# Optimization experiments

Hardware: AMD Instinct MI355X
Metric: run time of the kernel (lower is better)

Reference implementation:

```python
import jax, jax.numpy as jnp
import numpy as np

H = 512  # hidden/input size
T = 16384
CLAMP_MAX = 49688.0

def setup_inputs() -> dict:
    key = jax.random.key(0)
    ks = jax.random.split(key, 12)
    s = 0.05
    x = jax.random.normal(ks[0], (T, 1, H), dtype=jnp.float32)
    W_ih = jax.random.normal(ks[1], (4 * H, H), dtype=jnp.float32) * s
    W_hh = jax.random.normal(ks[2], (4 * H, H), dtype=jnp.float32) * s
    b_ih = jax.random.normal(ks[3], (4 * H,), dtype=jnp.float32) * s
    b_hh = jax.random.normal(ks[4], (4 * H,), dtype=jnp.float32) * s
    fc_w = jax.random.normal(ks[5], (128, H), dtype=jnp.float32) * s
    fc_b = jax.random.normal(ks[6], (128,), dtype=jnp.float32) * s
    fc1_w = jax.random.normal(ks[7], (16, 128), dtype=jnp.float32) * s
    fc1_b = jax.random.normal(ks[8], (16,), dtype=jnp.float32) * s
    fc2_w = jax.random.normal(ks[9], (37, 128), dtype=jnp.float32) * s
    fc2_b = jax.random.normal(ks[10], (37,), dtype=jnp.float32) * s
    return {"x": x, "W_ih": W_ih, "W_hh": W_hh, "b_ih": b_ih, "b_hh": b_hh,
            "fc_w": fc_w, "fc_b": fc_b, "fc1_w": fc1_w, "fc1_b": fc1_b,
            "fc2_w": fc2_w, "fc2_b": fc2_b}

def _lstm(x, W_ih, W_hh, b_ih, b_hh):
    # x: [T, 1, H] seq-major, batch=1. Precompute input contribution for all t.
    xf = x.reshape(-1, H)                       # [T, H]
    x_gates = xf @ W_ih.T + (b_ih + b_hh)       # [T, 4H]

    def step(carry, xg):
        h, c = carry                            # [H], [H]
        g = xg + W_hh @ h                       # [4H]
        i = jax.nn.sigmoid(g[:H])
        f = jax.nn.sigmoid(g[H:2 * H])
        gg = jnp.tanh(g[2 * H:3 * H])
        o = jax.nn.sigmoid(g[3 * H:])
        c = f * c + i * gg
        h = o * jnp.tanh(c)
        return (h, c), h

    h0 = jnp.zeros((H,), dtype=x.dtype)
    c0 = jnp.zeros((H,), dtype=x.dtype)
    _, hs = jax.lax.scan(step, (h0, c0), x_gates)  # hs: [T, H]
    return hs

def reference(x, W_ih, W_hh, b_ih, b_hh, fc_w, fc_b, fc1_w, fc1_b, fc2_w, fc2_b):
    hs = _lstm(x, W_ih, W_hh, b_ih, b_hh)       # [T, H]
    inter = hs @ fc_w.T + fc_b                  # [T, 128]
    action = jnp.clip(inter @ fc1_w.T + fc1_b, 0.0, CLAMP_MAX)  # [T, 16]
    obj = jnp.clip(inter @ fc2_w.T + fc2_b, 0.0, CLAMP_MAX)     # [T, 37]
    return (action, obj)
```

## Files before the change

kernel.cpp:

```cpp
#include <hip/hip_runtime.h>
#include <hip/hip_bf16.h>
#include <stdint.h>

#define T_LEN 16384
#define HDIM 512
#define G4 2048
#define CLAMP_MAXV 49688.0f

#define XG_OFF    0ull
#define HS_OFF    134217728ull
#define INTER_OFF 167772160ull
#define HREC_OFF  176160768ull
#define BSUM_OFF  176168960ull
#define WS_NEED   176177152ull

__global__ __launch_bounds__(256) void init_k(uint64_t* __restrict__ hrec,
                                              const float* __restrict__ b_ih,
                                              const float* __restrict__ b_hh,
                                              float* __restrict__ bsum) {
    int i = blockIdx.x * 256 + threadIdx.x;
    if (i < 1024) hrec[i] = 0ull;
    bsum[i] = b_ih[i] + b_hh[i];
}

__global__ __launch_bounds__(256) void gemm_abt(const float* __restrict__ A,
                                                const float* __restrict__ B,
                                                const float* __restrict__ bias,
                                                float* __restrict__ C,
                                                int N, int K) {
    __shared__ float As[16][68];
    __shared__ float Bs[16][68];
    const int tid = threadIdx.x;
    const int bm = blockIdx.x << 6, bn = blockIdx.y << 6;
    const int tx = tid & 15, ty = tid >> 4;
    const int lr = tid >> 2, lk = (tid & 3) << 2;
    float acc[4][4] = {};
    const float* Ap = A + (size_t)(bm + lr) * K + lk;
    const float* Bp = B + (size_t)(bn + lr) * K + lk;
    for (int kt = 0; kt < K; kt += 16) {
        float4 av = *(const float4*)(Ap + kt);
        float4 bv = *(const float4*)(Bp + kt);
        __syncthreads();
        As[lk + 0][lr] = av.x; As[lk + 1][lr] = av.y;
        As[lk + 2][lr] = av.z; As[lk + 3][lr] = av.w;
        Bs[lk + 0][lr] = bv.x; Bs[lk + 1][lr] = bv.y;
        Bs[lk + 2][lr] = bv.z; Bs[lk + 3][lr] = bv.w;
        __syncthreads();
#pragma unroll
        for (int kk = 0; kk < 16; ++kk) {
            float4 a4 = *(const float4*)&As[kk][ty << 2];
            float4 b4 = *(const float4*)&Bs[kk][tx << 2];
            acc[0][0] += a4.x * b4.x; acc[0][1] += a4.x * b4.y;
            acc[0][2] += a4.x * b4.z; acc[0][3] += a4.x * b4.w;
            acc[1][0] += a4.y * b4.x; acc[1][1] += a4.y * b4.y;
            acc[1][2] += a4.y * b4.z; acc[1][3] += a4.y * b4.w;
            acc[2][0] += a4.z * b4.x; acc[2][1] += a4.z * b4.y;
            acc[2][2] += a4.z * b4.z; acc[2][3] += a4.z * b4.w;
            acc[3][0] += a4.w * b4.x; acc[3][1] += a4.w * b4.y;
            acc[3][2] += a4.w * b4.z; acc[3][3] += a4.w * b4.w;
        }
    }
    const int col = bn + (tx << 2);
    float4 bv4 = *(const float4*)&bias[col];
#pragma unroll
    for (int i = 0; i < 4; ++i) {
        int row = bm + (ty << 2) + i;
        float4 o;
        o.x = acc[i][0] + bv4.x; o.y = acc[i][1] + bv4.y;
        o.z = acc[i][2] + bv4.z; o.w = acc[i][3] + bv4.w;
        *(float4*)&C[(size_t)row * N + col] = o;
    }
}

__global__ __launch_bounds__(512, 2) void lstm_scan(const float* __restrict__ W_hh,
                                                    const float* __restrict__ xg,
                                                    float* __restrict__ hs,
                                                    uint64_t* __restrict__ hrec) {
    __shared__ __align__(16) float h_lds[512];
    __shared__ float part[2][512];
    const int tid = threadIdx.x;
    const int wv = tid >> 6;
    const int lane = tid & 63;
    const int j = blockIdx.x;
    const int rowg = ((lane >> 4) << 9) | (j << 4) | (lane & 15);

    float4 w4[16];
    {
        const float4* wp = (const float4*)(W_hh + (size_t)rowg * HDIM + (wv << 6));
#pragma unroll
        for (int q = 0; q < 16; ++q) w4[q] = wp[q];
    }

    float c_reg = 0.f;
    for (int t = 0; t < T_LEN; ++t) {
        float xgv = 0.f;
        if (wv == 0) xgv = xg[(size_t)t * G4 + rowg];

        uint64_t* src = hrec + ((t & 1) << 9) + tid;
        uint64_t a0 = __hip_atomic_load(src, __ATOMIC_RELAXED, __HIP_MEMORY_SCOPE_AGENT);
        uint64_t a1 = __hip_atomic_load(src, __ATOMIC_RELAXED, __HIP_MEMORY_SCOPE_AGENT);
        int guard = 0;
        while ((uint32_t)(a0 >> 32) != (uint32_t)t && ++guard < (1 << 18)) {
            a0 = a1;
            a1 = __hip_atomic_load(src, __ATOMIC_RELAXED, __HIP_MEMORY_SCOPE_AGENT);
        }
        h_lds[tid] = __uint_as_float((uint32_t)a0);
        __builtin_amdgcn_wave_barrier();

        float ac0 = 0.f, ac1 = 0.f, ac2 = 0.f, ac3 = 0.f;
        const float* hp = h_lds + (wv << 6);
#pragma unroll
        for (int q = 0; q < 16; q += 4) {
            float4 h0 = *(const float4*)(hp + (q << 2));
            float4 h1 = *(const float4*)(hp + ((q + 1) << 2));
            float4 h2 = *(const float4*)(hp + ((q + 2) << 2));
            float4 h3 = *(const float4*)(hp + ((q + 3) << 2));
            ac0 += w4[q].x * h0.x + w4[q].y * h0.y + w4[q].z * h0.z + w4[q].w * h0.w;
            ac1 += w4[q + 1].x * h1.x + w4[q + 1].y * h1.y + w4[q + 1].z * h1.z + w4[q + 1].w * h1.w;
            ac2 += w4[q + 2].x * h2.x + w4[q + 2].y * h2.y + w4[q + 2].z * h2.z + w4[q + 2].w * h2.w;
            ac3 += w4[q + 3].x * h3.x + w4[q + 3].y * h3.y + w4[q + 3].z * h3.z + w4[q + 3].w * h3.w;
        }
        float v = (ac0 + ac1) + (ac2 + ac3);
        if (wv) part[t & 1][tid] = v;
        __syncthreads();

        if (wv == 0) {
            float g = xgv + v;
            const float* pp = part[t & 1];
#pragma unroll
            for (int ww = 1; ww < 8; ++ww) g += pp[(ww << 6) | lane];
            bool isg = (lane >= 32) && (lane < 48);
            float y = isg ? (g + g) : g;
            float s = 1.f / (1.f + __expf(-y));
            float a = isg ? (s + s - 1.f) : s;
            float fa = __shfl_down(a, 16);
            float ga = __shfl_down(a, 32);
            float oa = __shfl_down(a, 48);
            if (lane < 16) {
                c_reg = fa * c_reg + a * ga;
                float e2 = __expf(-2.f * c_reg);
                float hv = oa * (2.f / (1.f + e2) - 1.f);
                uint64_t pu = ((uint64_t)(uint32_t)(t + 1) << 32) |
                              (uint64_t)__float_as_uint(hv);
                __hip_atomic_store(hrec + (((t + 1) & 1) << 9) + (j << 4) + lane, pu,
                                   __ATOMIC_RELAXED, __HIP_MEMORY_SCOPE_AGENT);
                hs[(size_t)t * HDIM + (j << 4) + lane] = hv;
            }
        }
    }
}

__global__ __launch_bounds__(256) void heads_k(const float* __restrict__ inter,
                                               const float* __restrict__ fc1w,
                                               const float* __restrict__ fc1b,
                                               const float* __restrict__ fc2w,
                                               const float* __restrict__ fc2b,
                                               float* __restrict__ out) {
    __shared__ float it[64][128];
    __shared__ float wt[128][56];
    __shared__ float bl[56];
    const int tid = threadIdx.x;
    const int t0 = blockIdx.x << 6;
    for (int q = tid; q < 64 * 32; q += 256) {
        int r = q >> 5, c4 = q & 31;
        *(float4*)&it[r][c4 << 2] =
            *(const float4*)&inter[(size_t)(t0 + r) * 128 + (c4 << 2)];
    }
    for (int q = tid; q < 53 * 32; q += 256) {
        int r = q >> 5, c4 = q & 31;
        float4 v = (r < 16) ? ((const float4*)&fc1w[r * 128])[c4]
                            : ((const float4*)&fc2w[(r - 16) * 128])[c4];
        int k = c4 << 2;
        wt[k + 0][r] = v.x; wt[k + 1][r] = v.y; wt[k + 2][r] = v.z; wt[k + 3][r] = v.w;
    }
    if (tid < 53) bl[tid] = (tid < 16) ? fc1b[tid] : fc2b[tid - 16];
    __syncthreads();
    const int c = tid & 63, rg = tid >> 6;
    if (c < 53) {
        float b = bl[c];
        for (int rr = 0; rr < 16; ++rr) {
            int r = (rg << 4) + rr;
            float acc = b;
#pragma unroll 8
            for (int k = 0; k < 128; k += 4) {
                float4 iv = *(const float4*)&it[r][k];
                acc += iv.x * wt[k][c] + iv.y * wt[k + 1][c] +
                       iv.z * wt[k + 2][c] + iv.w * wt[k + 3][c];
            }
            acc = fminf(fmaxf(acc, 0.f), CLAMP_MAXV);
            int t = t0 + r;
            if (c < 16) out[(size_t)t * 16 + c] = acc;
            else        out[262144 + (size_t)t * 37 + (c - 16)] = acc;
        }
    }
}

extern "C" void kernel_launch(void* const* d_in, const int* in_sizes, int n_in,
                              void* d_out, int out_size, void* d_ws, size_t ws_size,
                              hipStream_t stream) {
    const float* x     = (const float*)d_in[0];
    const float* W_ih  = (const float*)d_in[1];
    const float* W_hh  = (const float*)d_in[2];
    const float* b_ih  = (const float*)d_in[3];
    const float* b_hh  = (const float*)d_in[4];
    const float* fc_w  = (const float*)d_in[5];
    const float* fc_b  = (const float*)d_in[6];
    const float* fc1_w = (const float*)d_in[7];
    const float* fc1_b = (const float*)d_in[8];
    const float* fc2_w = (const float*)d_in[9];
    const float* fc2_b = (const float*)d_in[10];

    if (ws_size < WS_NEED) return;

    char* ws = (char*)d_ws;
    float*    xg    = (float*)(ws + XG_OFF);
    float*    hs    = (float*)(ws + HS_OFF);
    float*    inter = (float*)(ws + INTER_OFF);
    uint64_t* hrec  = (uint64_t*)(ws + HREC_OFF);
    float*    bsum  = (float*)(ws + BSUM_OFF);
    float*    out   = (float*)d_out;

    hipLaunchKernelGGL(init_k, dim3(8), dim3(256), 0, stream, hrec, b_ih, b_hh, bsum);
    hipLaunchKernelGGL(gemm_abt, dim3(256, 32), dim3(256), 0, stream,
                       x, W_ih, bsum, xg, 2048, 512);
    hipLaunchKernelGGL(lstm_scan, dim3(32), dim3(512), 0, stream, W_hh, xg, hs, hrec);
    hipLaunchKernelGGL(gemm_abt, dim3(256, 2), dim3(256), 0, stream,
                       hs, fc_w, fc_b, inter, 128, 512);
    hipLaunchKernelGGL(heads_k, dim3(256), dim3(256), 0, stream,
                       inter, fc1_w, fc1_b, fc2_w, fc2_b, out);
}
```

Measured before the change: 23.12 ms.

## Prefetch xg via helper wave, batch hs stores, reduce partials with LDS atomics

Wave 1 now prefetches the input-gate rows two steps ahead into a double-buffered LDS slot, so wave 0 no longer waits on a global load in the serial recurrence. The hs writes move off wave 0: values are staged in LDS and written by wave 2 every four steps. The cross-wave partial sums are combined with LDS atomicAdd into a 64-entry buffer instead of wave 0 reading seven partials serially. This shortens the per-step critical path, at the cost of atomic contention on LDS and a possible ordering race on the staged hs buffer, which has no block barrier between wave 0's write and wave 2's read.

```diff
diff --git a/kernel.cpp b/kernel.cpp
--- a/kernel.cpp
+++ b/kernel.cpp
@@ -77,7 +77,9 @@
                                                     float* __restrict__ hs,
                                                     uint64_t* __restrict__ hrec) {
     __shared__ __align__(16) float h_lds[512];
-    __shared__ float part[2][512];
+    __shared__ float part[2][64];
+    __shared__ float xg_lds[2][64];
+    __shared__ float hv_lds[64];
     const int tid = threadIdx.x;
     const int wv = tid >> 6;
     const int lane = tid & 63;
@@ -91,11 +93,16 @@
         for (int q = 0; q < 16; ++q) w4[q] = wp[q];
     }
 
+    if (tid < 128) ((float*)part)[tid] = 0.f;
+    float xg_inflight = 0.f;
+    if (wv == 1) {
+        xg_lds[0][lane] = xg[rowg];
+        xg_inflight = xg[(size_t)G4 + rowg];
+    }
+    __syncthreads();
+
     float c_reg = 0.f;
     for (int t = 0; t < T_LEN; ++t) {
-        float xgv = 0.f;
-        if (wv == 0) xgv = xg[(size_t)t * G4 + rowg];
-
         uint64_t* src = hrec + ((t & 1) << 9) + tid;
         uint64_t a0 = __hip_atomic_load(src, __ATOMIC_RELAXED, __HIP_MEMORY_SCOPE_AGENT);
         uint64_t a1 = __hip_atomic_load(src, __ATOMIC_RELAXED, __HIP_MEMORY_SCOPE_AGENT);
@@ -106,6 +113,20 @@
         }
         h_lds[tid] = __uint_as_float((uint32_t)a0);
         __builtin_amdgcn_wave_barrier();
+
+        float xgv = 0.f;
+        if (wv == 0) {
+            xgv = xg_lds[t & 1][lane];
+        } else if (wv == 1) {
+            xg_lds[(t + 1) & 1][lane] = xg_inflight;
+            int i2 = (t + 2 < T_LEN) ? (t + 2) : (T_LEN - 1);
+            xg_inflight = xg[(size_t)i2 * G4 + rowg];
+        } else if (wv == 2) {
+            if ((t & 3) == 0 && t > 0) {
+                float hvv = hv_lds[lane];
+                hs[(size_t)(t - 4 + (lane >> 4)) * HDIM + (j << 4) + (lane & 15)] = hvv;
+            }
+        }
 
         float ac0 = 0.f, ac1 = 0.f, ac2 = 0.f, ac3 = 0.f;
         const float* hp = h_lds + (wv << 6);
@@ -121,14 +142,12 @@
             ac3 += w4[q + 3].x * h3.x + w4[q + 3].y * h3.y + w4[q + 3].z * h3.z + w4[q + 3].w * h3.w;
         }
         float v = (ac0 + ac1) + (ac2 + ac3);
-        if (wv) part[t & 1][tid] = v;
+        if (wv) atomicAdd(&part[t & 1][lane], v);
         __syncthreads();
 
         if (wv == 0) {
-            float g = xgv + v;
-            const float* pp = part[t & 1];
-#pragma unroll
-            for (int ww = 1; ww < 8; ++ww) g += pp[(ww << 6) | lane];
+            float g = xgv + v + part[t & 1][lane];
+            part[t & 1][lane] = 0.f;
             bool isg = (lane >= 32) && (lane < 48);
             float y = isg ? (g + g) : g;
             float s = 1.f / (1.f + __expf(-y));
@@ -140,13 +159,18 @@
                 c_reg = fa * c_reg + a * ga;
                 float e2 = __expf(-2.f * c_reg);
                 float hv = oa * (2.f / (1.f + e2) - 1.f);
+                hv_lds[((t & 3) << 4) | lane] = hv;
                 uint64_t pu = ((uint64_t)(uint32_t)(t + 1) << 32) |
                               (uint64_t)__float_as_uint(hv);
                 __hip_atomic_store(hrec + (((t + 1) & 1) << 9) + (j << 4) + lane, pu,
                                    __ATOMIC_RELAXED, __HIP_MEMORY_SCOPE_AGENT);
-                hs[(size_t)t * HDIM + (j << 4) + lane] = hv;
             }
         }
+    }
+    __syncthreads();
+    if (wv == 2) {
+        float hvv = hv_lds[lane];
+        hs[(size_t)(T_LEN - 4 + (lane >> 4)) * HDIM + (j << 4) + (lane & 15)] = hvv;
     }
 }
 
```

After: 32.61 ms. 41.0% more time.

## Co-locate LSTM scan blocks on one XCD and exchange state through L2

Applied to the files above, without the earlier changes.

The recurrent scan now launches 256 blocks. It reads the XCC ID so that the first 32 blocks landing on one chiplet claim roles, and the rest exit. Once co-located, the per-step hidden-state exchange uses sc0 loads and stores that stay in the shared L2 instead of agent-scope atomics that go to device-coherent memory. A runtime probe with grid barriers checks that L2 visibility works and falls back to atomics if it does not. The next step's xg value is also prefetched during the current step. This adds startup barrier overhead and relies on undocumented cache-coherence behaviour within an XCD.

```diff
diff --git a/kernel.cpp b/kernel.cpp
--- a/kernel.cpp
+++ b/kernel.cpp
@@ -14,13 +14,31 @@
 #define BSUM_OFF  176168960ull
 #define WS_NEED   176177152ull
 
+#define SCAN_BLOCKS 32
+#define XCC_ID_ENC (20 | (0 << 6) | ((32 - 1) << 11))
+
+__device__ __forceinline__ uint64_t l2_load_u64(const uint64_t* p) {
+    uint64_t v;
+    asm volatile("global_load_dwordx2 %0, %1, off sc0\n\ts_waitcnt vmcnt(0)"
+                 : "=&v"(v) : "v"(p) : "memory");
+    return v;
+}
+__device__ __forceinline__ void l2_store_u64(uint64_t* p, uint64_t v) {
+    asm volatile("global_store_dwordx2 %0, %1, off sc0"
+                 :: "v"(p), "v"(v) : "memory");
+}
+
 __global__ __launch_bounds__(256) void init_k(uint64_t* __restrict__ hrec,
                                               const float* __restrict__ b_ih,
                                               const float* __restrict__ b_hh,
-                                              float* __restrict__ bsum) {
+                                              float* __restrict__ bsum,
+                                              uint32_t* __restrict__ ctrl,
+                                              uint64_t* __restrict__ probe) {
     int i = blockIdx.x * 256 + threadIdx.x;
     if (i < 1024) hrec[i] = 0ull;
     bsum[i] = b_ih[i] + b_hh[i];
+    if (i < 16) ctrl[i] = (i == 8) ? 0xFFFFFFFFu : 0u;
+    else if (i < 16 + 512) probe[i - 16] = 0ull;
 }
 
 __global__ __launch_bounds__(256) void gemm_abt(const float* __restrict__ A,
@@ -75,34 +93,123 @@
 __global__ __launch_bounds__(512, 2) void lstm_scan(const float* __restrict__ W_hh,
                                                     const float* __restrict__ xg,
                                                     float* __restrict__ hs,
-                                                    uint64_t* __restrict__ hrec) {
+                                                    uint64_t* __restrict__ hrec,
+                                                    uint32_t* __restrict__ ctrl,
+                                                    uint64_t* __restrict__ probe) {
     __shared__ __align__(16) float h_lds[512];
     __shared__ float part[2][512];
+    __shared__ int role_sh;
+    __shared__ int fail_sh;
+    __shared__ int l2_sh;
     const int tid = threadIdx.x;
     const int wv = tid >> 6;
     const int lane = tid & 63;
-    const int j = blockIdx.x;
+
+    if (tid == 0) {
+        uint32_t xcd = ((uint32_t)__builtin_amdgcn_s_getreg(XCC_ID_ENC)) & 7u;
+        uint32_t slot = __hip_atomic_fetch_add(&ctrl[xcd], 1u,
+                            __ATOMIC_RELAXED, __HIP_MEMORY_SCOPE_AGENT);
+        int role = -1;
+        if (slot < (uint32_t)SCAN_BLOCKS) {
+            if (slot == SCAN_BLOCKS - 1) {
+                uint32_t exp = 0xFFFFFFFFu;
+                __hip_atomic_compare_exchange_strong(&ctrl[8], &exp, xcd,
+                    __ATOMIC_RELAXED, __ATOMIC_RELAXED, __HIP_MEMORY_SCOPE_AGENT);
+            }
+            uint32_t w; int g = 0;
+            do {
+                w = __hip_atomic_load(&ctrl[8], __ATOMIC_RELAXED,
+                                      __HIP_MEMORY_SCOPE_AGENT);
+            } while (w == 0xFFFFFFFFu && ++g < (1 << 22));
+            if (w == xcd) role = (int)slot;
+        }
+        role_sh = role;
+    }
+    __syncthreads();
+    const int j = role_sh;
+    if (j < 0) return;
+
+    auto pbar = [&](uint32_t epoch) {
+        if (tid == 0) {
+            asm volatile("s_waitcnt vmcnt(0)" ::: "memory");
+            __hip_atomic_fetch_add(&ctrl[9], 1u, __ATOMIC_RELAXED,
+                                   __HIP_MEMORY_SCOPE_AGENT);
+            uint32_t tgt = (uint32_t)SCAN_BLOCKS * epoch, v; int g = 0;
+            do {
+                v = __hip_atomic_load(&ctrl[9], __ATOMIC_RELAXED,
+                                      __HIP_MEMORY_SCOPE_AGENT);
+            } while (v < tgt && ++g < (1 << 22));
+        }
+        __syncthreads();
+    };
+
+    if (tid == 0) fail_sh = 0;
+    __syncthreads();
+    if (wv == 0 && lane < 16)
+        l2_store_u64(&probe[(j << 4) | lane],
+                     ((uint64_t)(0xABC00000u | (uint32_t)j) << 32) | 0x5EEDull);
+    pbar(1);
+    {
+        uint32_t want = 0xABC00000u | (uint32_t)(tid >> 4);
+        uint64_t u; int g = 0;
+        do { u = l2_load_u64(&probe[tid]); }
+        while ((uint32_t)(u >> 32) != want && ++g < (1 << 15));
+        if ((uint32_t)(u >> 32) != want) atomicOr(&fail_sh, 1);
+    }
+    pbar(2);
+    if (wv == 0 && lane < 16)
+        l2_store_u64(&probe[(j << 4) | lane],
+                     ((uint64_t)(0xDEF00000u | (uint32_t)j) << 32) | 0xBEEFull);
+    pbar(3);
+    {
+        uint32_t want = 0xDEF00000u | (uint32_t)(tid >> 4);
+        uint64_t u; int g = 0;
+        do { u = l2_load_u64(&probe[tid]); }
+        while ((uint32_t)(u >> 32) != want && ++g < (1 << 13));
+        if ((uint32_t)(u >> 32) != want) atomicOr(&fail_sh, 1);
+    }
+    __syncthreads();
+    if (tid == 0 && fail_sh)
+        __hip_atomic_fetch_add(&ctrl[10], 1u, __ATOMIC_RELAXED,
+                               __HIP_MEMORY_SCOPE_AGENT);
+    pbar(4);
+    if (tid == 0)
+        l2_sh = (__hip_atomic_load(&ctrl[10], __ATOMIC_RELAXED,
+                                   __HIP_MEMORY_SCOPE_AGENT) == 0u) ? 1 : 0;
+    __syncthreads();
+    const bool use_l2 = (l2_sh != 0);
+
     const int rowg = ((lane >> 4) << 9) | (j << 4) | (lane & 15);
-
     float4 w4[16];
     {
         const float4* wp = (const float4*)(W_hh + (size_t)rowg * HDIM + (wv << 6));
 #pragma unroll
         for (int q = 0; q < 16; ++q) w4[q] = wp[q];
     }
+    float xg_next = 0.f;
+    if (wv == 0) xg_next = xg[rowg];
 
     float c_reg = 0.f;
     for (int t = 0; t < T_LEN; ++t) {
-        float xgv = 0.f;
-        if (wv == 0) xgv = xg[(size_t)t * G4 + rowg];
+        float xgv = xg_next;
 
         uint64_t* src = hrec + ((t & 1) << 9) + tid;
-        uint64_t a0 = __hip_atomic_load(src, __ATOMIC_RELAXED, __HIP_MEMORY_SCOPE_AGENT);
-        uint64_t a1 = __hip_atomic_load(src, __ATOMIC_RELAXED, __HIP_MEMORY_SCOPE_AGENT);
-        int guard = 0;
-        while ((uint32_t)(a0 >> 32) != (uint32_t)t && ++guard < (1 << 18)) {
-            a0 = a1;
-            a1 = __hip_atomic_load(src, __ATOMIC_RELAXED, __HIP_MEMORY_SCOPE_AGENT);
+        uint64_t a0;
+        if (use_l2) {
+            a0 = l2_load_u64(src);
+            int g = 0;
+            while ((uint32_t)(a0 >> 32) != (uint32_t)t && ++g < (1 << 18)) {
+                __builtin_amdgcn_s_sleep(1);
+                a0 = l2_load_u64(src);
+            }
+        } else {
+            a0 = __hip_atomic_load(src, __ATOMIC_RELAXED, __HIP_MEMORY_SCOPE_AGENT);
+            uint64_t a1 = __hip_atomic_load(src, __ATOMIC_RELAXED, __HIP_MEMORY_SCOPE_AGENT);
+            int g = 0;
+            while ((uint32_t)(a0 >> 32) != (uint32_t)t && ++g < (1 << 18)) {
+                a0 = a1;
+                a1 = __hip_atomic_load(src, __ATOMIC_RELAXED, __HIP_MEMORY_SCOPE_AGENT);
+            }
         }
         h_lds[tid] = __uint_as_float((uint32_t)a0);
         __builtin_amdgcn_wave_barrier();
@@ -142,10 +249,13 @@
                 float hv = oa * (2.f / (1.f + e2) - 1.f);
                 uint64_t pu = ((uint64_t)(uint32_t)(t + 1) << 32) |
                               (uint64_t)__float_as_uint(hv);
-                __hip_atomic_store(hrec + (((t + 1) & 1) << 9) + (j << 4) + lane, pu,
-                                   __ATOMIC_RELAXED, __HIP_MEMORY_SCOPE_AGENT);
+                uint64_t* dst = hrec + (((t + 1) & 1) << 9) + (j << 4) + lane;
+                if (use_l2) l2_store_u64(dst, pu);
+                else __hip_atomic_store(dst, pu, __ATOMIC_RELAXED,
+                                        __HIP_MEMORY_SCOPE_AGENT);
                 hs[(size_t)t * HDIM + (j << 4) + lane] = hv;
             }
+            if (t + 1 < T_LEN) xg_next = xg[(size_t)(t + 1) * G4 + rowg];
         }
     }
 }
@@ -218,12 +328,16 @@
     float*    inter = (float*)(ws + INTER_OFF);
     uint64_t* hrec  = (uint64_t*)(ws + HREC_OFF);
     float*    bsum  = (float*)(ws + BSUM_OFF);
+    uint32_t* ctrl  = (uint32_t*)(ws + INTER_OFF);
+    uint64_t* probe = (uint64_t*)(ws + INTER_OFF + 64);
     float*    out   = (float*)d_out;
 
-    hipLaunchKernelGGL(init_k, dim3(8), dim3(256), 0, stream, hrec, b_ih, b_hh, bsum);
+    hipLaunchKernelGGL(init_k, dim3(8), dim3(256), 0, stream,
+                       hrec, b_ih, b_hh, bsum, ctrl, probe);
     hipLaunchKernelGGL(gemm_abt, dim3(256, 32), dim3(256), 0, stream,
                        x, W_ih, bsum, xg, 2048, 512);
-    hipLaunchKernelGGL(lstm_scan, dim3(32), dim3(512), 0, stream, W_hh, xg, hs, hrec);
+    hipLaunchKernelGGL(lstm_scan, dim3(256), dim3(512), 0, stream,
+                       W_hh, xg, hs, hrec, ctrl, probe);
     hipLaunchKernelGGL(gemm_abt, dim3(256, 2), dim3(256), 0, stream,
                        hs, fc_w, fc_b, inter, 128, 512);
     hipLaunchKernelGGL(heads_k, dim3(256), dim3(256), 0, stream,
```

Measured after the change: 26.37 ms. 14.0% more time.
